# Performance work log

Measured on AMD Instinct MI355X. Metric: run time of the kernel, lower is better.

## Reference

```python
import jax, jax.numpy as jnp
import numpy as np

DIM = 64
N_EMBED = 512


def setup_inputs() -> dict:
    key = jax.random.key(0)
    k_x, k_e = jax.random.split(key)
    x = jax.random.normal(k_x, (32, 64, 64, DIM), dtype=jnp.float32)
    # codebook buffer: embed has shape [dim, n_embed] as in the torch module
    embed = jax.random.normal(k_e, (DIM, N_EMBED), dtype=jnp.float32)
    return {"x": x, "embed": embed}


def reference(x, embed):
    # x: [B, H, W, dim]; embed: [dim, n_embed]
    dim = embed.shape[0]
    flat = x.reshape(-1, dim)  # [N, dim]
    # squared euclidean distance (same argmin as torch.cdist's euclid dist)
    # d2[n, k] = ||flat[n]||^2 - 2 flat[n].embed[:,k] + ||embed[:,k]||^2
    d2 = (
        jnp.sum(flat * flat, axis=1, keepdims=True)
        - 2.0 * (flat @ embed)
        + jnp.sum(embed * embed, axis=0)[None, :]
    )  # [N, n_embed]
    embed_ind = jnp.argmin(d2, axis=1)  # [N]
    embed_ind = embed_ind.reshape(x.shape[:-1])  # [B, H, W]
    # embedding lookup from embed.T ([n_embed, dim])
    quantize = jnp.take(embed.T, embed_ind, axis=0)  # [B, H, W, dim]
    diff = jnp.mean(jnp.square(jax.lax.stop_gradient(quantize) - x))
    # straight-through estimator
    quantize_st = x + jax.lax.stop_gradient(quantize - x)
    return quantize_st, diff, embed_ind
```

## Files before the change

### kernel.cpp

```cpp
#include <hip/hip_runtime.h>


#define DIM      64
#define NCODE    512
#define NVEC     (32 * 64 * 64)
#define WAVES    4
#define BLK      256
#define NCT      16
#define CHUNK_DW 3072

typedef unsigned int u32;
typedef __attribute__((ext_vector_type(8)))  short bf16x8;
typedef __attribute__((ext_vector_type(16))) float f32x16;

#define GLOAD_LDS16(gp, lp)                                                      \
  __builtin_amdgcn_global_load_lds(                                              \
      (const __attribute__((address_space(1))) u32*)(gp),                        \
      (__attribute__((address_space(3))) u32*)(lp), 16, 0, 0)

__device__ __forceinline__ void split3(float v, u32& h, u32& m, u32& lo) {
    const u32 u = __float_as_uint(v);
    h = u >> 16;
    const float r1 = v - __uint_as_float(u & 0xFFFF0000u);
    const u32 u1 = __float_as_uint(r1);
    m = u1 >> 16;
    const float r2 = r1 - __uint_as_float(u1 & 0xFFFF0000u);
    lo = __float_as_uint(r2) >> 16;
}

__global__ void vq_prep(const float* __restrict__ embed,
                        u32* __restrict__ bfrag,
                        float* __restrict__ et,
                        float* __restrict__ norms,
                        float* __restrict__ out) {
    const int gid = blockIdx.x * BLK + threadIdx.x;
    const int c = gid >> 3, g = gid & 7;
    const int s = g >> 1, kh = g & 1;

    float v[8];
    double ns = 0.0;
    #pragma unroll
    for (int j = 0; j < 8; ++j) {
        v[j] = embed[(16 * s + 8 * kh + j) * NCODE + c];
        ns += (double)v[j] * (double)v[j];
    }
    ns += __shfl_xor(ns, 1, 64);
    ns += __shfl_xor(ns, 2, 64);
    ns += __shfl_xor(ns, 4, 64);
    if (g == 0) norms[c] = (float)ns;

    u32 wH[4], wM[4], wL[4];
    #pragma unroll
    for (int q = 0; q < 4; ++q) {
        u32 h0, m0, l0, h1, m1, l1;
        split3(v[2 * q], h0, m0, l0);
        split3(v[2 * q + 1], h1, m1, l1);
        wH[q] = h0 | (h1 << 16);
        wM[q] = m0 | (m1 << 16);
        wL[q] = l0 | (l1 << 16);
    }
    const int ct = c >> 5, lb = (c & 31) + 32 * kh;
    u32* base = bfrag + ct * CHUNK_DW;
    *reinterpret_cast<uint4*>(base + (0 * 4 + s) * 256 + lb * 4) =
        make_uint4(wH[0], wH[1], wH[2], wH[3]);
    *reinterpret_cast<uint4*>(base + (1 * 4 + s) * 256 + lb * 4) =
        make_uint4(wM[0], wM[1], wM[2], wM[3]);
    *reinterpret_cast<uint4*>(base + (2 * 4 + s) * 256 + lb * 4) =
        make_uint4(wL[0], wL[1], wL[2], wL[3]);

    float* ep = et + c * DIM + 16 * s + 8 * kh;
    *reinterpret_cast<float4*>(ep)     = make_float4(v[0], v[1], v[2], v[3]);
    *reinterpret_cast<float4*>(ep + 4) = make_float4(v[4], v[5], v[6], v[7]);

    if (gid == 0) out[(size_t)NVEC * DIM] = 0.0f;
}

__global__ __launch_bounds__(BLK, 4) void vq_main(
        const float* __restrict__ x,
        const u32* __restrict__ bfrag,
        const float* __restrict__ et,
        const float* __restrict__ norms,
        float* __restrict__ out) {
    __shared__ __align__(16) u32 lbuf[2][CHUNK_DW];
    __shared__ float lnorm[NCODE];
    __shared__ int sbk[WAVES][32];
    __shared__ float red[WAVES];

    const int tid = threadIdx.x;
    const int wid = tid >> 6, l = tid & 63;
    const int rl = l & 31, kh = l >> 5;
    const int n0 = (blockIdx.x * WAVES + wid) * 32;

    {
        const u32* gsrc = bfrag + wid * 256 + (l << 2);
        u32* lp = &lbuf[0][wid * 256];
        GLOAD_LDS16(gsrc, lp);
        GLOAD_LDS16(gsrc + 1024, lp + 1024);
        GLOAD_LDS16(gsrc + 2048, lp + 2048);
    }
    for (int i = tid; i < NCODE; i += BLK) lnorm[i] = norms[i];

    bf16x8 afr[3][4];
    {
        const float* xp = x + (size_t)(n0 + rl) * DIM + kh * 8;
        #pragma unroll
        for (int s = 0; s < 4; ++s) {
            const float4 va = *reinterpret_cast<const float4*>(xp + 16 * s);
            const float4 vb = *reinterpret_cast<const float4*>(xp + 16 * s + 4);
            const float v[8] = {va.x, va.y, va.z, va.w, vb.x, vb.y, vb.z, vb.w};
            #pragma unroll
            for (int q = 0; q < 4; ++q) {
                u32 h0, m0, l0, h1, m1, l1;
                split3(v[2 * q], h0, m0, l0);
                split3(v[2 * q + 1], h1, m1, l1);
                afr[0][s][2 * q] = (short)h0;  afr[0][s][2 * q + 1] = (short)h1;
                afr[1][s][2 * q] = (short)m0;  afr[1][s][2 * q + 1] = (short)m1;
                afr[2][s][2 * q] = (short)l0;  afr[2][s][2 * q + 1] = (short)l1;
            }
        }
    }

    float best[16];
    int bk[16];
    #pragma unroll
    for (int r = 0; r < 16; ++r) { best[r] = __builtin_inff(); bk[r] = 0; }

    for (int ct = 0; ct < NCT; ++ct) {
        const int cur = ct & 1;
        if (ct + 1 < NCT) {
            const u32* gsrc = bfrag + (ct + 1) * CHUNK_DW + wid * 256 + (l << 2);
            u32* lp = &lbuf[cur ^ 1][wid * 256];
            GLOAD_LDS16(gsrc, lp);
            GLOAD_LDS16(gsrc + 1024, lp + 1024);
            GLOAD_LDS16(gsrc + 2048, lp + 2048);
            asm volatile("s_waitcnt vmcnt(3)" ::: "memory");
        } else {
            asm volatile("s_waitcnt vmcnt(0)" ::: "memory");
        }
        asm volatile("s_barrier" ::: "memory");

        f32x16 acc;
        #pragma unroll
        for (int r = 0; r < 16; ++r) acc[r] = 0.0f;

        const int l4 = l << 2;
        #pragma unroll
        for (int s = 0; s < 4; ++s) {
            const bf16x8 bh = *reinterpret_cast<const bf16x8*>(&lbuf[cur][(0 * 4 + s) * 256 + l4]);
            const bf16x8 bm = *reinterpret_cast<const bf16x8*>(&lbuf[cur][(1 * 4 + s) * 256 + l4]);
            const bf16x8 bl = *reinterpret_cast<const bf16x8*>(&lbuf[cur][(2 * 4 + s) * 256 + l4]);
            acc = __builtin_amdgcn_mfma_f32_32x32x16_bf16(afr[0][s], bh, acc, 0, 0, 0);
            acc = __builtin_amdgcn_mfma_f32_32x32x16_bf16(afr[0][s], bm, acc, 0, 0, 0);
            acc = __builtin_amdgcn_mfma_f32_32x32x16_bf16(afr[1][s], bh, acc, 0, 0, 0);
            acc = __builtin_amdgcn_mfma_f32_32x32x16_bf16(afr[1][s], bm, acc, 0, 0, 0);
            acc = __builtin_amdgcn_mfma_f32_32x32x16_bf16(afr[0][s], bl, acc, 0, 0, 0);
            acc = __builtin_amdgcn_mfma_f32_32x32x16_bf16(afr[2][s], bh, acc, 0, 0, 0);
        }

        const int col = ct * 32 + rl;
        const float nrm = lnorm[col];
        #pragma unroll
        for (int r = 0; r < 16; ++r) {
            const float sc = fmaf(-2.0f, acc[r], nrm);
            if (sc < best[r]) { best[r] = sc; bk[r] = col; }
        }

        asm volatile("s_barrier" ::: "memory");
    }

    #pragma unroll
    for (int off = 1; off <= 16; off <<= 1) {
        #pragma unroll
        for (int r = 0; r < 16; ++r) {
            const float ob = __shfl_xor(best[r], off, 64);
            const int obk  = __shfl_xor(bk[r], off, 64);
            if (ob < best[r] || (ob == best[r] && obk < bk[r])) { best[r] = ob; bk[r] = obk; }
        }
    }
    if (rl == 0) {
        #pragma unroll
        for (int r = 0; r < 16; ++r) sbk[wid][(r & 3) + 8 * (r >> 2) + 4 * kh] = bk[r];
    }

    float dp = 0.0f;
    const int rsub = l >> 4;
    const int dcol = (l & 15) * 4;
    #pragma unroll
    for (int i = 0; i < 8; ++i) {
        const int row = i * 4 + rsub;
        const int k = sbk[wid][row];
        const float4 q  = *reinterpret_cast<const float4*>(et + k * DIM + dcol);
        const float4 xv = *reinterpret_cast<const float4*>(x + (size_t)(n0 + row) * DIM + dcol);
        *reinterpret_cast<float4*>(out + (size_t)(n0 + row) * DIM + dcol) = q;
        const float d0 = q.x - xv.x, d1 = q.y - xv.y, d2 = q.z - xv.z, d3 = q.w - xv.w;
        dp = fmaf(d0, d0, dp); dp = fmaf(d1, d1, dp);
        dp = fmaf(d2, d2, dp); dp = fmaf(d3, d3, dp);
    }
    if (l < 32) out[(size_t)NVEC * DIM + 1 + n0 + l] = (float)sbk[wid][l];

    #pragma unroll
    for (int off = 32; off >= 1; off >>= 1) dp += __shfl_down(dp, off, 64);
    if (l == 0) red[wid] = dp;
    __syncthreads();
    if (tid == 0) {
        const float s = (red[0] + red[1]) + (red[2] + red[3]);
        atomicAdd(out + (size_t)NVEC * DIM, s * (1.0f / ((float)NVEC * (float)DIM)));
    }
}

extern "C" void kernel_launch(void* const* d_in, const int* in_sizes, int n_in,
                              void* d_out, int out_size, void* d_ws, size_t ws_size,
                              hipStream_t stream) {
    const float* x     = (const float*)d_in[0];
    const float* embed = (const float*)d_in[1];
    float* out = (float*)d_out;

    u32* bfrag   = (u32*)d_ws;
    float* et    = (float*)d_ws + NCT * CHUNK_DW;
    float* norms = et + (size_t)NCODE * DIM;

    vq_prep<<<16, BLK, 0, stream>>>(embed, bfrag, et, norms, out);
    vq_main<<<NVEC / (WAVES * 32), BLK, 0, stream>>>(x, bfrag, et, norms, out);
}
```

Before: 134.4 us.

## Load codebook fragments directly from global memory instead of LDS double-buffering

Drops the LDS double-buffered staging of codebook B-fragments and norms. Each wave now reads its bf16 fragments and the norm straight from global memory (L2/L1-cached) into registers every tile, so the per-tile block barriers go away. Launch bounds drop from 4 to 3 blocks per CU, which gives more registers for the 12 fragment vectors. The cost is redundant global/cache traffic from every wave and load latency that is no longer hidden by an explicit prefetch.

```diff
diff --git a/kernel.cpp b/kernel.cpp
--- a/kernel.cpp
+++ b/kernel.cpp
@@ -12,11 +12,6 @@
 typedef unsigned int u32;
 typedef __attribute__((ext_vector_type(8)))  short bf16x8;
 typedef __attribute__((ext_vector_type(16))) float f32x16;
-
-#define GLOAD_LDS16(gp, lp)                                                      \
-  __builtin_amdgcn_global_load_lds(                                              \
-      (const __attribute__((address_space(1))) u32*)(gp),                        \
-      (__attribute__((address_space(3))) u32*)(lp), 16, 0, 0)
 
 __device__ __forceinline__ void split3(float v, u32& h, u32& m, u32& lo) {
     const u32 u = __float_as_uint(v);
@@ -53,7 +48,7 @@
     #pragma unroll
     for (int q = 0; q < 4; ++q) {
         u32 h0, m0, l0, h1, m1, l1;
-        split3(v[2 * q], h0, m0, l0);
+        split3(v[2 * q],     h0, m0, l0);
         split3(v[2 * q + 1], h1, m1, l1);
         wH[q] = h0 | (h1 << 16);
         wM[q] = m0 | (m1 << 16);
@@ -75,14 +70,12 @@
     if (gid == 0) out[(size_t)NVEC * DIM] = 0.0f;
 }
 
-__global__ __launch_bounds__(BLK, 4) void vq_main(
+__global__ __launch_bounds__(BLK, 3) void vq_main(
         const float* __restrict__ x,
         const u32* __restrict__ bfrag,
         const float* __restrict__ et,
         const float* __restrict__ norms,
         float* __restrict__ out) {
-    __shared__ __align__(16) u32 lbuf[2][CHUNK_DW];
-    __shared__ float lnorm[NCODE];
     __shared__ int sbk[WAVES][32];
     __shared__ float red[WAVES];
 
@@ -90,15 +83,6 @@
     const int wid = tid >> 6, l = tid & 63;
     const int rl = l & 31, kh = l >> 5;
     const int n0 = (blockIdx.x * WAVES + wid) * 32;
-
-    {
-        const u32* gsrc = bfrag + wid * 256 + (l << 2);
-        u32* lp = &lbuf[0][wid * 256];
-        GLOAD_LDS16(gsrc, lp);
-        GLOAD_LDS16(gsrc + 1024, lp + 1024);
-        GLOAD_LDS16(gsrc + 2048, lp + 2048);
-    }
-    for (int i = tid; i < NCODE; i += BLK) lnorm[i] = norms[i];
 
     bf16x8 afr[3][4];
     {
@@ -111,7 +95,7 @@
             #pragma unroll
             for (int q = 0; q < 4; ++q) {
                 u32 h0, m0, l0, h1, m1, l1;
-                split3(v[2 * q], h0, m0, l0);
+                split3(v[2 * q],     h0, m0, l0);
                 split3(v[2 * q + 1], h1, m1, l1);
                 afr[0][s][2 * q] = (short)h0;  afr[0][s][2 * q + 1] = (short)h1;
                 afr[1][s][2 * q] = (short)m0;  afr[1][s][2 * q + 1] = (short)m1;
@@ -125,47 +109,38 @@
     #pragma unroll
     for (int r = 0; r < 16; ++r) { best[r] = __builtin_inff(); bk[r] = 0; }
 
+    const u32* fb = bfrag + (l << 2);
     for (int ct = 0; ct < NCT; ++ct) {
-        const int cur = ct & 1;
-        if (ct + 1 < NCT) {
-            const u32* gsrc = bfrag + (ct + 1) * CHUNK_DW + wid * 256 + (l << 2);
-            u32* lp = &lbuf[cur ^ 1][wid * 256];
-            GLOAD_LDS16(gsrc, lp);
-            GLOAD_LDS16(gsrc + 1024, lp + 1024);
-            GLOAD_LDS16(gsrc + 2048, lp + 2048);
-            asm volatile("s_waitcnt vmcnt(3)" ::: "memory");
-        } else {
-            asm volatile("s_waitcnt vmcnt(0)" ::: "memory");
+        const u32* tb = fb + ct * CHUNK_DW;
+        bf16x8 b[3][4];
+        #pragma unroll
+        for (int s = 0; s < 4; ++s) {
+            b[0][s] = *reinterpret_cast<const bf16x8*>(tb + (0 * 4 + s) * 256);
+            b[1][s] = *reinterpret_cast<const bf16x8*>(tb + (1 * 4 + s) * 256);
+            b[2][s] = *reinterpret_cast<const bf16x8*>(tb + (2 * 4 + s) * 256);
         }
-        asm volatile("s_barrier" ::: "memory");
+        const float nrm = norms[ct * 32 + rl];
 
         f32x16 acc;
         #pragma unroll
         for (int r = 0; r < 16; ++r) acc[r] = 0.0f;
 
-        const int l4 = l << 2;
         #pragma unroll
         for (int s = 0; s < 4; ++s) {
-            const bf16x8 bh = *reinterpret_cast<const bf16x8*>(&lbuf[cur][(0 * 4 + s) * 256 + l4]);
-            const bf16x8 bm = *reinterpret_cast<const bf16x8*>(&lbuf[cur][(1 * 4 + s) * 256 + l4]);
-            const bf16x8 bl = *reinterpret_cast<const bf16x8*>(&lbuf[cur][(2 * 4 + s) * 256 + l4]);
-            acc = __builtin_amdgcn_mfma_f32_32x32x16_bf16(afr[0][s], bh, acc, 0, 0, 0);
-            acc = __builtin_amdgcn_mfma_f32_32x32x16_bf16(afr[0][s], bm, acc, 0, 0, 0);
-            acc = __builtin_amdgcn_mfma_f32_32x32x16_bf16(afr[1][s], bh, acc, 0, 0, 0);
-            acc = __builtin_amdgcn_mfma_f32_32x32x16_bf16(afr[1][s], bm, acc, 0, 0, 0);
-            acc = __builtin_amdgcn_mfma_f32_32x32x16_bf16(afr[0][s], bl, acc, 0, 0, 0);
-            acc = __builtin_amdgcn_mfma_f32_32x32x16_bf16(afr[2][s], bh, acc, 0, 0, 0);
+            acc = __builtin_amdgcn_mfma_f32_32x32x16_bf16(afr[0][s], b[0][s], acc, 0, 0, 0);
+            acc = __builtin_amdgcn_mfma_f32_32x32x16_bf16(afr[0][s], b[1][s], acc, 0, 0, 0);
+            acc = __builtin_amdgcn_mfma_f32_32x32x16_bf16(afr[1][s], b[0][s], acc, 0, 0, 0);
+            acc = __builtin_amdgcn_mfma_f32_32x32x16_bf16(afr[1][s], b[1][s], acc, 0, 0, 0);
+            acc = __builtin_amdgcn_mfma_f32_32x32x16_bf16(afr[0][s], b[2][s], acc, 0, 0, 0);
+            acc = __builtin_amdgcn_mfma_f32_32x32x16_bf16(afr[2][s], b[0][s], acc, 0, 0, 0);
         }
 
         const int col = ct * 32 + rl;
-        const float nrm = lnorm[col];
         #pragma unroll
         for (int r = 0; r < 16; ++r) {
             const float sc = fmaf(-2.0f, acc[r], nrm);
             if (sc < best[r]) { best[r] = sc; bk[r] = col; }
         }
-
-        asm volatile("s_barrier" ::: "memory");
     }
 
     #pragma unroll
```

Result: slower. 145.5 us (+8.2%).
